# Optimization experiments

Hardware: AMD Instinct MI355X
Metric: run time of the kernel (lower is better)

## Reference

```python
import jax, jax.numpy as jnp
import numpy as np

N_HEAD, N, F_IN, F_OUT = 8, 4096, 128, 128


def setup_inputs() -> dict:
    key = jax.random.key(0)
    k1, k2, k3, k4 = jax.random.split(key, 4)
    return {
        "h": jax.random.normal(k1, (N, F_IN), dtype=jnp.float32),
        "w": jax.random.normal(k2, (N_HEAD, F_IN, F_OUT), dtype=jnp.float32) * 0.1,
        "a_src": jax.random.normal(k3, (N_HEAD, F_OUT, 1), dtype=jnp.float32) * 0.1,
        "a_dst": jax.random.normal(k4, (N_HEAD, F_OUT, 1), dtype=jnp.float32) * 0.1,
        "bias": jnp.zeros((F_OUT,), dtype=jnp.float32),
        "idx": 0,
    }


def reference(h, w, a_src, a_dst, bias, idx):
    # h: [n, f_in], w: [H, f_in, f_out] -> h_prime: [H, n, f_out]
    h_prime = jnp.einsum("ni,hio->hno", h, w)
    # per-node scalar scores per head: [H, n]
    attn_src = jnp.einsum("hno,ho->hn", h_prime, a_src[..., 0])
    attn_dst = jnp.einsum("hno,ho->hn", h_prime, a_dst[..., 0])
    # dense additive attention: [H, n, n] (src broadcast over cols + dst over rows)
    attn = attn_src[:, :, None] + attn_dst[:, None, :]
    attn = jax.nn.leaky_relu(attn, negative_slope=0.2)
    attn = jax.nn.softmax(attn, axis=-1)
    # dropout is identity in eval mode
    out = jnp.einsum("hnm,hmo->hno", attn, h_prime)  # [H, n, f_out]
    return out.mean(axis=0) + bias  # [n, f_out]
```

## Files before the change

### kernel.cpp

```cpp
#include <hip/hip_runtime.h>
#include <math.h>

#define NH 8
#define NN 4096
#define FF 128
#define SEG 32
#define NSEG (NN / SEG)

typedef unsigned long long u64;

__global__ __launch_bounds__(256) void k1_gemm(
    const float* __restrict__ h, const float* __restrict__ w,
    const float* __restrict__ a_src, const float* __restrict__ a_dst,
    float* __restrict__ hp, float* __restrict__ attn_src,
    float* __restrict__ attn_dst) {
  __shared__ float sw[32 * 128];
  __shared__ float shT[32 * 32];
  const int head = blockIdx.y;
  const int r0 = blockIdx.x * 32;
  const int tid = threadIdx.x;
  const int ty = tid >> 5;
  const int tx = tid & 31;

  float acc[4][4];
  #pragma unroll
  for (int i = 0; i < 4; ++i)
    #pragma unroll
    for (int j = 0; j < 4; ++j) acc[i][j] = 0.f;

  const float4* wg = reinterpret_cast<const float4*>(w + (size_t)head * 128 * 128);
  const float4* hg = reinterpret_cast<const float4*>(h);

  for (int kc = 0; kc < 4; ++kc) {
    const int k0 = kc * 32;
    __syncthreads();
    #pragma unroll
    for (int it = 0; it < 4; ++it) {
      int q = tid + it * 256;
      int krow = q >> 5, c4 = q & 31;
      float4 v = wg[(size_t)(k0 + krow) * 32 + c4];
      float* dst = &sw[krow * 128 + c4 * 4];
      dst[0] = v.x; dst[1] = v.y; dst[2] = v.z; dst[3] = v.w;
    }
    {
      int row = tid >> 3, k4 = tid & 7;
      float4 v = hg[(size_t)(r0 + row) * 32 + (k0 >> 2) + k4];
      #pragma unroll
      for (int j = 0; j < 4; ++j) {
        int kl = k4 * 4 + j;
        int rsw = row ^ (((kl >> 2) & 7) << 2);
        shT[kl * 32 + rsw] = (&v.x)[j];
      }
    }
    __syncthreads();
    #pragma unroll 8
    for (int kk = 0; kk < 32; ++kk) {
      float4 a4 = *reinterpret_cast<const float4*>(
          &shT[kk * 32 + ((ty ^ ((kk >> 2) & 7)) << 2)]);
      float4 b4 = *reinterpret_cast<const float4*>(&sw[kk * 128 + tx * 4]);
      #pragma unroll
      for (int ri = 0; ri < 4; ++ri) {
        float av = (&a4.x)[ri];
        acc[ri][0] += av * b4.x;
        acc[ri][1] += av * b4.y;
        acc[ri][2] += av * b4.z;
        acc[ri][3] += av * b4.w;
      }
    }
  }

  const int rbase = r0 + ty * 4;
  float4* hp4 = reinterpret_cast<float4*>(hp);
  #pragma unroll
  for (int ri = 0; ri < 4; ++ri) {
    hp4[((size_t)(head * NN + rbase + ri)) * 32 + tx] =
        make_float4(acc[ri][0], acc[ri][1], acc[ri][2], acc[ri][3]);
  }
  float4 As = reinterpret_cast<const float4*>(a_src + head * FF)[tx];
  float4 Ad = reinterpret_cast<const float4*>(a_dst + head * FF)[tx];
  #pragma unroll
  for (int ri = 0; ri < 4; ++ri) {
    float sA = acc[ri][0] * As.x + acc[ri][1] * As.y + acc[ri][2] * As.z +
               acc[ri][3] * As.w;
    float sD = acc[ri][0] * Ad.x + acc[ri][1] * Ad.y + acc[ri][2] * Ad.z +
               acc[ri][3] * Ad.w;
    #pragma unroll
    for (int m = 1; m < 32; m <<= 1) {
      sA += __shfl_xor(sA, m);
      sD += __shfl_xor(sD, m);
    }
    if (tx == 0) {
      attn_src[head * NN + rbase + ri] = sA;
      attn_dst[head * NN + rbase + ri] = sD;
    }
  }
}

__global__ __launch_bounds__(256) void k2a_localsort(
    const float* __restrict__ adst, u64* __restrict__ runs) {
  __shared__ u64 sk[512];
  const int head = blockIdx.y, chunk = blockIdx.x, tid = threadIdx.x;
  const int base = head * NN + chunk * 512;
  for (int i = tid; i < 512; i += 256) {
    unsigned ub = __float_as_uint(adst[base + i]);
    unsigned u = (ub & 0x80000000u) ? ~ub : (ub | 0x80000000u);
    sk[i] = ((u64)u << 32) | (unsigned)(chunk * 512 + i);
  }
  __syncthreads();
  for (int k = 2; k <= 512; k <<= 1) {
    for (int j = k >> 1; j > 0; j >>= 1) {
      for (int t = tid; t < 512; t += 256) {
        int ixj = t ^ j;
        if (ixj > t) {
          u64 a = sk[t], b = sk[ixj];
          bool up = ((t & k) == 0);
          if (up ? (a > b) : (a < b)) { sk[t] = b; sk[ixj] = a; }
        }
      }
      __syncthreads();
    }
  }
  for (int i = tid; i < 512; i += 256) runs[base + i] = sk[i];
}

template <int L, bool FINAL>
__global__ __launch_bounds__(256) void k2m(
    const u64* __restrict__ src, u64* __restrict__ dst,
    float* __restrict__ dsort, int* __restrict__ permd) {
  const int head = blockIdx.y;
  const int i = (blockIdx.x * 256 + threadIdx.x) * 4;
  const u64* S = src + head * NN;
  const int region = i / (2 * L), q0 = i % (2 * L);
  const u64* A = S + region * 2 * L;
  const u64* B = A + L;
  int lo = q0 > L ? q0 - L : 0, hi = q0 < L ? q0 : L;
  while (lo < hi) {
    int mid = (lo + hi) >> 1;
    if (A[mid] < B[q0 - 1 - mid]) lo = mid + 1; else hi = mid;
  }
  int a = lo, b = q0 - lo;
  #pragma unroll
  for (int t = 0; t < 4; ++t) {
    u64 va = a < L ? A[a] : ~0ULL;
    u64 vb = b < L ? B[b] : ~0ULL;
    u64 v;
    if (va < vb) { v = va; ++a; } else { v = vb; ++b; }
    const int q = region * 2 * L + q0 + t;
    if (FINAL) {
      unsigned u = (unsigned)(v >> 32);
      unsigned ub = (u & 0x80000000u) ? (u ^ 0x80000000u) : ~u;
      dsort[head * NN + q] = __uint_as_float(ub);
      permd[head * NN + q] = (int)(v & 0xffffffffu);
    } else {
      dst[head * NN + q] = v;
    }
  }
}

__global__ __launch_bounds__(256) void k3_segsum(
    const float* __restrict__ hp, const float* __restrict__ dsort,
    const int* __restrict__ permd, float* __restrict__ segs,
    float* __restrict__ segz) {
  __shared__ float se0[SEG], se1[SEG];
  __shared__ int sp[SEG];
  __shared__ float comb[2 * FF];
  const int head = blockIdx.y, seg = blockIdx.x;
  const int tid = threadIdx.x;
  const int o = tid & 127, jh = tid >> 7;
  const int sbse = head * NN + seg * SEG;
  if (tid < SEG) {
    float dv = dsort[sbse + tid];
    se0[tid] = expf(0.2f * dv);
    sp[tid] = permd[sbse + tid];
  } else if (tid < 2 * SEG) {
    int t = tid - SEG;
    se1[t] = expf(dsort[sbse + t]);
  }
  __syncthreads();
  const float* hph = hp + (size_t)head * NN * FF;
  float a0 = 0.f, a1 = 0.f;
  #pragma unroll
  for (int u = 0; u < SEG / 2; ++u) {
    int jj = u * 2 + jh;
    float hv = hph[(size_t)sp[jj] * FF + o];
    a0 += se0[jj] * hv;
    a1 += se1[jj] * hv;
  }
  if (jh == 1) {
    comb[o] = a0;
    comb[FF + o] = a1;
  }
  __syncthreads();
  if (jh == 0) {
    a0 += comb[o];
    a1 += comb[FF + o];
    size_t base = ((size_t)(head * NSEG + seg)) * 2 * FF;
    segs[base + o] = a0;
    segs[base + FF + o] = a1;
    if (o == 0) {
      float zz0 = 0.f, zz1 = 0.f;
      #pragma unroll
      for (int j = 0; j < SEG; ++j) { zz0 += se0[j]; zz1 += se1[j]; }
      segz[(head * NSEG + seg) * 2 + 0] = zz0;
      segz[(head * NSEG + seg) * 2 + 1] = zz1;
    }
  }
}

__global__ __launch_bounds__(256) void k4_thresh(
    const float* __restrict__ attn_src, const float* __restrict__ dsort,
    int* __restrict__ tpos) {
  const int i = blockIdx.x * 256 + threadIdx.x;
  const int head = i >> 12, n = i & (NN - 1);
  const float thr = -attn_src[head * NN + n];
  const float* dp = dsort + head * NN;
  int lo = 0, hi = NN;
  while (lo < hi) {
    int mid = (lo + hi) >> 1;
    if (dp[mid] <= thr) lo = mid + 1; else hi = mid;
  }
  tpos[i] = lo;
}

__global__ __launch_bounds__(128) void k5_prefix(
    const float* __restrict__ hp, const float* __restrict__ dsort,
    const int* __restrict__ permd, const float* __restrict__ segs,
    const float* __restrict__ segz, float* __restrict__ PF,
    float* __restrict__ PFz) {
  __shared__ float se0[SEG], se1[SEG];
  __shared__ int sp[SEG];
  const int head = blockIdx.y, seg = blockIdx.x;
  const int o = threadIdx.x;
  const int sbse = head * NN + seg * SEG;
  if (o < SEG) {
    float dv = dsort[sbse + o];
    se0[o] = expf(0.2f * dv);
    sp[o] = permd[sbse + o];
  } else if (o < 2 * SEG) {
    int t = o - SEG;
    se1[t] = expf(dsort[sbse + t]);
  }
  __syncthreads();
  float r0 = 0.f, r1 = 0.f, z0 = 0.f, z1 = 0.f;
  const float* sbase = segs + ((size_t)head * NSEG) * 2 * FF;
  #pragma unroll 8
  for (int k = 0; k < seg; ++k) {
    r0 += sbase[(size_t)k * 2 * FF + o];
    r1 += sbase[(size_t)k * 2 * FF + FF + o];
  }
  #pragma unroll 8
  for (int k = 0; k < seg; ++k) {
    z0 += segz[(head * NSEG + k) * 2 + 0];
    z1 += segz[(head * NSEG + k) * 2 + 1];
  }
  const float* hph = hp + (size_t)head * NN * FF;
  #pragma unroll 8
  for (int jj = 0; jj < SEG; ++jj) {
    int j = seg * SEG + jj;
    float hv = hph[(size_t)sp[jj] * FF + o];
    float e0 = se0[jj], e1 = se1[jj];
    r0 += e0 * hv;
    r1 += e1 * hv;
    z0 += e0;
    z1 += e1;
    size_t pb = ((size_t)(head * NN + j)) * 2 * FF;
    PF[pb + o] = r0;
    PF[pb + FF + o] = r1;
    if (o == 0) {
      PFz[(head * NN + j) * 2 + 0] = z0;
      PFz[(head * NN + j) * 2 + 1] = z1;
    }
  }
}

__global__ __launch_bounds__(128) void k6_out(
    const float* __restrict__ attn_src, const int* __restrict__ tpos,
    const float* __restrict__ PF, const float* __restrict__ PFz,
    const float* __restrict__ bias, float* __restrict__ out) {
  const int n = blockIdx.x, o = threadIdx.x;
  float acc = 0.f;
  #pragma unroll
  for (int head = 0; head < NH; ++head) {
    float s = attn_src[head * NN + n];
    int t = tpos[head * NN + n];
    size_t tb = ((size_t)(head * NN + NN - 1)) * 2 * FF;
    float TotA = PF[tb + FF + o];
    float z1tot = PFz[(head * NN + NN - 1) * 2 + 1];
    float B = 0.f, P1 = 0.f, z0p = 0.f, z1p = 0.f;
    if (t > 0) {
      size_t pb = ((size_t)(head * NN + t - 1)) * 2 * FF;
      B = PF[pb + o];
      P1 = PF[pb + FF + o];
      z0p = PFz[(head * NN + t - 1) * 2 + 0];
      z1p = PFz[(head * NN + t - 1) * 2 + 1];
    }
    float e02s = expf(0.2f * s), es = expf(s);
    float den = e02s * z0p + es * (z1tot - z1p);
    acc += (e02s * B + es * (TotA - P1)) / den;
  }
  out[(size_t)n * FF + o] = 0.125f * acc + bias[o];
}

extern "C" void kernel_launch(void* const* d_in, const int* in_sizes, int n_in,
                              void* d_out, int out_size, void* d_ws,
                              size_t ws_size, hipStream_t stream) {
  const float* h = (const float*)d_in[0];
  const float* w = (const float*)d_in[1];
  const float* a_src = (const float*)d_in[2];
  const float* a_dst = (const float*)d_in[3];
  const float* bias = (const float*)d_in[4];
  float* out = (float*)d_out;

  char* ws = (char*)d_ws;
  size_t off = 0;
  auto alloc = [&](size_t bytes) -> void* {
    void* p = ws + off;
    off += (bytes + 255) & ~(size_t)255;
    return p;
  };
  float* hp = (float*)alloc((size_t)NH * NN * FF * 4);
  float* asrc = (float*)alloc((size_t)NH * NN * 4);
  float* adst = (float*)alloc((size_t)NH * NN * 4);
  float* dsort = (float*)alloc((size_t)NH * NN * 4);
  int* permd = (int*)alloc((size_t)NH * NN * 4);
  int* tpos = (int*)alloc((size_t)NH * NN * 4);
  float* segs = (float*)alloc((size_t)NH * NSEG * 2 * FF * 4);
  float* segz = (float*)alloc((size_t)NH * NSEG * 2 * 4);
  float* PF = (float*)alloc((size_t)NH * NN * 2 * FF * 4);
  float* PFz = (float*)alloc((size_t)NH * NN * 2 * 4);
  u64* sbuf0 = (u64*)alloc((size_t)NH * NN * 8);
  u64* sbuf1 = (u64*)alloc((size_t)NH * NN * 8);
  (void)ws_size;

  k1_gemm<<<dim3(NN / 32, NH), 256, 0, stream>>>(h, w, a_src, a_dst, hp, asrc,
                                                 adst);
  k2a_localsort<<<dim3(8, NH), 256, 0, stream>>>(adst, sbuf0);
  k2m<512, false><<<dim3(4, NH), 256, 0, stream>>>(sbuf0, sbuf1, nullptr,
                                                   nullptr);
  k2m<1024, false><<<dim3(4, NH), 256, 0, stream>>>(sbuf1, sbuf0, nullptr,
                                                    nullptr);
  k2m<2048, true><<<dim3(4, NH), 256, 0, stream>>>(sbuf0, nullptr, dsort,
                                                   permd);
  k3_segsum<<<dim3(NSEG, NH), 256, 0, stream>>>(hp, dsort, permd, segs, segz);
  k4_thresh<<<NH * NN / 256, 256, 0, stream>>>(asrc, dsort, tpos);
  k5_prefix<<<dim3(NSEG, NH), 128, 0, stream>>>(hp, dsort, permd, segs, segz,
                                                PF, PFz);
  k6_out<<<NN, 128, 0, stream>>>(asrc, tpos, PF, PFz, bias, out);
}
```

Before: 162.2 us.

## Compute scores via folded W·a vectors and fuse sorted-order GEMM into segment sums

Attention scores are now computed as h·(W a) using precomputed per-head vectors, so the full h·W projection is no longer needed before the sort. The projection GEMM moves after the sort and runs on h rows gathered in sorted order. It is fused with the per-segment weighted sums and writes h' in sorted layout, so the prefix kernel reads rows contiguously instead of gathering through the permutation. This drops one pass over h' and the scattered gathers, in exchange for extra small launches and a gathered h load inside the GEMM.

```diff
diff --git a/kernel.cpp b/kernel.cpp
--- a/kernel.cpp
+++ b/kernel.cpp
@@ -9,91 +9,66 @@
 
 typedef unsigned long long u64;
 
-__global__ __launch_bounds__(256) void k1_gemm(
-    const float* __restrict__ h, const float* __restrict__ w,
-    const float* __restrict__ a_src, const float* __restrict__ a_dst,
-    float* __restrict__ hp, float* __restrict__ attn_src,
+__global__ __launch_bounds__(128) void kA_va(
+    const float* __restrict__ w, const float* __restrict__ a_src,
+    const float* __restrict__ a_dst, float* __restrict__ va_s,
+    float* __restrict__ va_d) {
+  __shared__ float as[FF], ad[FF];
+  const int head = blockIdx.x, i = threadIdx.x;
+  as[i] = a_src[head * FF + i];
+  ad[i] = a_dst[head * FF + i];
+  __syncthreads();
+  const float4* wr = reinterpret_cast<const float4*>(w + (size_t)head * FF * FF +
+                                                     (size_t)i * FF);
+  float s = 0.f, d = 0.f;
+  #pragma unroll 8
+  for (int q = 0; q < 32; ++q) {
+    float4 v = wr[q];
+    s += v.x * as[q * 4] + v.y * as[q * 4 + 1] + v.z * as[q * 4 + 2] +
+         v.w * as[q * 4 + 3];
+    d += v.x * ad[q * 4] + v.y * ad[q * 4 + 1] + v.z * ad[q * 4 + 2] +
+         v.w * ad[q * 4 + 3];
+  }
+  va_s[head * FF + i] = s;
+  va_d[head * FF + i] = d;
+}
+
+__global__ __launch_bounds__(256) void kB_scores(
+    const float* __restrict__ h, const float* __restrict__ va_s,
+    const float* __restrict__ va_d, float* __restrict__ attn_src,
     float* __restrict__ attn_dst) {
-  __shared__ float sw[32 * 128];
-  __shared__ float shT[32 * 32];
-  const int head = blockIdx.y;
+  __shared__ float sh[32 * 132];
+  __shared__ float vs[NH * 132], vd[NH * 132];
   const int r0 = blockIdx.x * 32;
   const int tid = threadIdx.x;
-  const int ty = tid >> 5;
-  const int tx = tid & 31;
-
-  float acc[4][4];
-  #pragma unroll
-  for (int i = 0; i < 4; ++i)
-    #pragma unroll
-    for (int j = 0; j < 4; ++j) acc[i][j] = 0.f;
-
-  const float4* wg = reinterpret_cast<const float4*>(w + (size_t)head * 128 * 128);
   const float4* hg = reinterpret_cast<const float4*>(h);
-
-  for (int kc = 0; kc < 4; ++kc) {
-    const int k0 = kc * 32;
-    __syncthreads();
-    #pragma unroll
-    for (int it = 0; it < 4; ++it) {
-      int q = tid + it * 256;
-      int krow = q >> 5, c4 = q & 31;
-      float4 v = wg[(size_t)(k0 + krow) * 32 + c4];
-      float* dst = &sw[krow * 128 + c4 * 4];
-      dst[0] = v.x; dst[1] = v.y; dst[2] = v.z; dst[3] = v.w;
-    }
-    {
-      int row = tid >> 3, k4 = tid & 7;
-      float4 v = hg[(size_t)(r0 + row) * 32 + (k0 >> 2) + k4];
-      #pragma unroll
-      for (int j = 0; j < 4; ++j) {
-        int kl = k4 * 4 + j;
-        int rsw = row ^ (((kl >> 2) & 7) << 2);
-        shT[kl * 32 + rsw] = (&v.x)[j];
-      }
-    }
-    __syncthreads();
-    #pragma unroll 8
-    for (int kk = 0; kk < 32; ++kk) {
-      float4 a4 = *reinterpret_cast<const float4*>(
-          &shT[kk * 32 + ((ty ^ ((kk >> 2) & 7)) << 2)]);
-      float4 b4 = *reinterpret_cast<const float4*>(&sw[kk * 128 + tx * 4]);
-      #pragma unroll
-      for (int ri = 0; ri < 4; ++ri) {
-        float av = (&a4.x)[ri];
-        acc[ri][0] += av * b4.x;
-        acc[ri][1] += av * b4.y;
-        acc[ri][2] += av * b4.z;
-        acc[ri][3] += av * b4.w;
-      }
-    }
-  }
-
-  const int rbase = r0 + ty * 4;
-  float4* hp4 = reinterpret_cast<float4*>(hp);
-  #pragma unroll
-  for (int ri = 0; ri < 4; ++ri) {
-    hp4[((size_t)(head * NN + rbase + ri)) * 32 + tx] =
-        make_float4(acc[ri][0], acc[ri][1], acc[ri][2], acc[ri][3]);
-  }
-  float4 As = reinterpret_cast<const float4*>(a_src + head * FF)[tx];
-  float4 Ad = reinterpret_cast<const float4*>(a_dst + head * FF)[tx];
-  #pragma unroll
-  for (int ri = 0; ri < 4; ++ri) {
-    float sA = acc[ri][0] * As.x + acc[ri][1] * As.y + acc[ri][2] * As.z +
-               acc[ri][3] * As.w;
-    float sD = acc[ri][0] * Ad.x + acc[ri][1] * Ad.y + acc[ri][2] * Ad.z +
-               acc[ri][3] * Ad.w;
-    #pragma unroll
-    for (int m = 1; m < 32; m <<= 1) {
-      sA += __shfl_xor(sA, m);
-      sD += __shfl_xor(sD, m);
-    }
-    if (tx == 0) {
-      attn_src[head * NN + rbase + ri] = sA;
-      attn_dst[head * NN + rbase + ri] = sD;
-    }
-  }
+  #pragma unroll
+  for (int it = 0; it < 4; ++it) {
+    int q = tid + it * 256;
+    int row = q >> 5, c4 = q & 31;
+    float4 v = hg[(size_t)(r0 + row) * 32 + c4];
+    float* dst = &sh[row * 132 + c4 * 4];
+    dst[0] = v.x; dst[1] = v.y; dst[2] = v.z; dst[3] = v.w;
+  }
+  for (int q = tid; q < NH * FF; q += 256) {
+    int hd = q >> 7, k = q & 127;
+    vs[hd * 132 + k] = va_s[q];
+    vd[hd * 132 + k] = va_d[q];
+  }
+  __syncthreads();
+  const int row = tid >> 3, head = tid & 7;
+  float s = 0.f, d = 0.f;
+  const float* hr = &sh[row * 132];
+  const float* vsp = &vs[head * 132];
+  const float* vdp = &vd[head * 132];
+  #pragma unroll 8
+  for (int k = 0; k < FF; ++k) {
+    float hv = hr[k];
+    s += hv * vsp[k];
+    d += hv * vdp[k];
+  }
+  attn_src[head * NN + r0 + row] = s;
+  attn_dst[head * NN + r0 + row] = d;
 }
 
 __global__ __launch_bounds__(256) void k2a_localsort(
@@ -157,53 +132,101 @@
   }
 }
 
-__global__ __launch_bounds__(256) void k3_segsum(
-    const float* __restrict__ hp, const float* __restrict__ dsort,
-    const int* __restrict__ permd, float* __restrict__ segs,
+__global__ __launch_bounds__(256) void kD_gemm_seg(
+    const float* __restrict__ h, const float* __restrict__ w,
+    const float* __restrict__ dsort, const int* __restrict__ permd,
+    float* __restrict__ hs, float* __restrict__ segs,
     float* __restrict__ segz) {
+  __shared__ float sw[32 * 128];
+  __shared__ float hA[32 * 128];
+  __shared__ float red[2 * 8 * 128];
   __shared__ float se0[SEG], se1[SEG];
   __shared__ int sp[SEG];
-  __shared__ float comb[2 * FF];
   const int head = blockIdx.y, seg = blockIdx.x;
   const int tid = threadIdx.x;
-  const int o = tid & 127, jh = tid >> 7;
-  const int sbse = head * NN + seg * SEG;
+  const int ty = tid >> 5, tx = tid & 31;
   if (tid < SEG) {
-    float dv = dsort[sbse + tid];
+    float dv = dsort[head * NN + seg * SEG + tid];
     se0[tid] = expf(0.2f * dv);
-    sp[tid] = permd[sbse + tid];
-  } else if (tid < 2 * SEG) {
-    int t = tid - SEG;
-    se1[t] = expf(dsort[sbse + t]);
-  }
-  __syncthreads();
-  const float* hph = hp + (size_t)head * NN * FF;
-  float a0 = 0.f, a1 = 0.f;
-  #pragma unroll
-  for (int u = 0; u < SEG / 2; ++u) {
-    int jj = u * 2 + jh;
-    float hv = hph[(size_t)sp[jj] * FF + o];
-    a0 += se0[jj] * hv;
-    a1 += se1[jj] * hv;
-  }
-  if (jh == 1) {
-    comb[o] = a0;
-    comb[FF + o] = a1;
-  }
-  __syncthreads();
-  if (jh == 0) {
-    a0 += comb[o];
-    a1 += comb[FF + o];
+    se1[tid] = expf(dv);
+    sp[tid] = permd[head * NN + seg * SEG + tid];
+  }
+  __syncthreads();
+  const float4* hg = reinterpret_cast<const float4*>(h);
+  #pragma unroll
+  for (int it = 0; it < 4; ++it) {
+    int row = tid >> 3, c4 = (tid & 7) + it * 8;
+    float4 v = hg[(size_t)sp[row] * 32 + c4];
+    float* dst = &hA[row * 128 + c4 * 4];
+    dst[0] = v.x; dst[1] = v.y; dst[2] = v.z; dst[3] = v.w;
+  }
+  float acc[4][4];
+  #pragma unroll
+  for (int i = 0; i < 4; ++i)
+    #pragma unroll
+    for (int j = 0; j < 4; ++j) acc[i][j] = 0.f;
+  const float4* wg = reinterpret_cast<const float4*>(w + (size_t)head * FF * FF);
+  for (int kc = 0; kc < 4; ++kc) {
+    const int k0 = kc * 32;
+    __syncthreads();
+    #pragma unroll
+    for (int it = 0; it < 4; ++it) {
+      int q = tid + it * 256;
+      int krow = q >> 5, c4 = q & 31;
+      float4 v = wg[(size_t)(k0 + krow) * 32 + c4];
+      float* dst = &sw[krow * 128 + c4 * 4];
+      dst[0] = v.x; dst[1] = v.y; dst[2] = v.z; dst[3] = v.w;
+    }
+    __syncthreads();
+    #pragma unroll 8
+    for (int kk = 0; kk < 32; ++kk) {
+      float4 b4 = *reinterpret_cast<const float4*>(&sw[kk * 128 + tx * 4]);
+      #pragma unroll
+      for (int ri = 0; ri < 4; ++ri) {
+        float av = hA[(ty * 4 + ri) * 128 + k0 + kk];
+        acc[ri][0] += av * b4.x;
+        acc[ri][1] += av * b4.y;
+        acc[ri][2] += av * b4.z;
+        acc[ri][3] += av * b4.w;
+      }
+    }
+  }
+  float4* hs4 = reinterpret_cast<float4*>(hs);
+  #pragma unroll
+  for (int ri = 0; ri < 4; ++ri) {
+    hs4[((size_t)(head * NN + seg * SEG + ty * 4 + ri)) * 32 + tx] =
+        make_float4(acc[ri][0], acc[ri][1], acc[ri][2], acc[ri][3]);
+  }
+  #pragma unroll
+  for (int c = 0; c < 4; ++c) {
+    float p0 = 0.f, p1 = 0.f;
+    #pragma unroll
+    for (int ri = 0; ri < 4; ++ri) {
+      int R = ty * 4 + ri;
+      p0 += se0[R] * acc[ri][c];
+      p1 += se1[R] * acc[ri][c];
+    }
+    red[ty * 128 + tx * 4 + c] = p0;
+    red[1024 + ty * 128 + tx * 4 + c] = p1;
+  }
+  __syncthreads();
+  if (tid < FF) {
+    float a0 = 0.f, a1 = 0.f;
+    #pragma unroll
+    for (int g = 0; g < 8; ++g) {
+      a0 += red[g * 128 + tid];
+      a1 += red[1024 + g * 128 + tid];
+    }
     size_t base = ((size_t)(head * NSEG + seg)) * 2 * FF;
-    segs[base + o] = a0;
-    segs[base + FF + o] = a1;
-    if (o == 0) {
-      float zz0 = 0.f, zz1 = 0.f;
-      #pragma unroll
-      for (int j = 0; j < SEG; ++j) { zz0 += se0[j]; zz1 += se1[j]; }
-      segz[(head * NSEG + seg) * 2 + 0] = zz0;
-      segz[(head * NSEG + seg) * 2 + 1] = zz1;
-    }
+    segs[base + tid] = a0;
+    segs[base + FF + tid] = a1;
+  }
+  if (tid == 0) {
+    float z0 = 0.f, z1 = 0.f;
+    #pragma unroll
+    for (int j = 0; j < SEG; ++j) { z0 += se0[j]; z1 += se1[j]; }
+    segz[(head * NSEG + seg) * 2 + 0] = z0;
+    segz[(head * NSEG + seg) * 2 + 1] = z1;
   }
 }
 
@@ -222,23 +245,17 @@
   tpos[i] = lo;
 }
 
-__global__ __launch_bounds__(128) void k5_prefix(
-    const float* __restrict__ hp, const float* __restrict__ dsort,
-    const int* __restrict__ permd, const float* __restrict__ segs,
-    const float* __restrict__ segz, float* __restrict__ PF,
-    float* __restrict__ PFz) {
+__global__ __launch_bounds__(128) void kF_prefix(
+    const float* __restrict__ hs, const float* __restrict__ dsort,
+    const float* __restrict__ segs, const float* __restrict__ segz,
+    float* __restrict__ PF, float* __restrict__ PFz) {
   __shared__ float se0[SEG], se1[SEG];
-  __shared__ int sp[SEG];
   const int head = blockIdx.y, seg = blockIdx.x;
   const int o = threadIdx.x;
-  const int sbse = head * NN + seg * SEG;
   if (o < SEG) {
-    float dv = dsort[sbse + o];
+    float dv = dsort[head * NN + seg * SEG + o];
     se0[o] = expf(0.2f * dv);
-    sp[o] = permd[sbse + o];
-  } else if (o < 2 * SEG) {
-    int t = o - SEG;
-    se1[t] = expf(dsort[sbse + t]);
+    se1[o] = expf(dv);
   }
   __syncthreads();
   float r0 = 0.f, r1 = 0.f, z0 = 0.f, z1 = 0.f;
@@ -253,11 +270,11 @@
     z0 += segz[(head * NSEG + k) * 2 + 0];
     z1 += segz[(head * NSEG + k) * 2 + 1];
   }
-  const float* hph = hp + (size_t)head * NN * FF;
+  const float* hrow = hs + ((size_t)(head * NN + seg * SEG)) * FF + o;
   #pragma unroll 8
   for (int jj = 0; jj < SEG; ++jj) {
     int j = seg * SEG + jj;
-    float hv = hph[(size_t)sp[jj] * FF + o];
+    float hv = hrow[(size_t)jj * FF];
     float e0 = se0[jj], e1 = se1[jj];
     r0 += e0 * hv;
     r1 += e1 * hv;
@@ -318,7 +335,9 @@
     off += (bytes + 255) & ~(size_t)255;
     return p;
   };
-  float* hp = (float*)alloc((size_t)NH * NN * FF * 4);
+  float* hs = (float*)alloc((size_t)NH * NN * FF * 4);
+  float* va_s = (float*)alloc((size_t)NH * FF * 4);
+  float* va_d = (float*)alloc((size_t)NH * FF * 4);
   float* asrc = (float*)alloc((size_t)NH * NN * 4);
   float* adst = (float*)alloc((size_t)NH * NN * 4);
   float* dsort = (float*)alloc((size_t)NH * NN * 4);
@@ -330,10 +349,10 @@
   float* PFz = (float*)alloc((size_t)NH * NN * 2 * 4);
   u64* sbuf0 = (u64*)alloc((size_t)NH * NN * 8);
   u64* sbuf1 = (u64*)alloc((size_t)NH * NN * 8);
-  (void)ws_size;
-
-  k1_gemm<<<dim3(NN / 32, NH), 256, 0, stream>>>(h, w, a_src, a_dst, hp, asrc,
-                                                 adst);
+  (void)ws_size; (void)in_sizes; (void)n_in;
+
+  kA_va<<<NH, 128, 0, stream>>>(w, a_src, a_dst, va_s, va_d);
+  kB_scores<<<NN / 32, 256, 0, stream>>>(h, va_s, va_d, asrc, adst);
   k2a_localsort<<<dim3(8, NH), 256, 0, stream>>>(adst, sbuf0);
   k2m<512, false><<<dim3(4, NH), 256, 0, stream>>>(sbuf0, sbuf1, nullptr,
                                                    nullptr);
@@ -341,9 +360,10 @@
                                                     nullptr);
   k2m<2048, true><<<dim3(4, NH), 256, 0, stream>>>(sbuf0, nullptr, dsort,
                                                    permd);
-  k3_segsum<<<dim3(NSEG, NH), 256, 0, stream>>>(hp, dsort, permd, segs, segz);
+  kD_gemm_seg<<<dim3(NSEG, NH), 256, 0, stream>>>(h, w, dsort, permd, hs, segs,
+                                                  segz);
   k4_thresh<<<NH * NN / 256, 256, 0, stream>>>(asrc, dsort, tpos);
-  k5_prefix<<<dim3(NSEG, NH), 128, 0, stream>>>(hp, dsort, permd, segs, segz,
-                                                PF, PFz);
+  kF_prefix<<<dim3(NSEG, NH), 128, 0, stream>>>(hs, dsort, segs, segz, PF,
+                                                PFz);
   k6_out<<<NN, 128, 0, stream>>>(asrc, tpos, PF, PFz, bias, out);
 }
```

Result: no change. 164.3 us (+1.3%).
